# Optimization experiments

Measured on AMD Instinct MI355X. Metric: run time of the kernel, lower is better.

## Reference

```python
import jax, jax.numpy as jnp
import numpy as np

N, G, P = 512, 11560, 2000
E_SG, E_GP, E_PP = 1000000, 200000, 50000
HID, HEADS, L = 192, 4, 2
C = HID // HEADS
NQ, OUT = 20, 128
EPS = 1e-5


def setup_inputs():
    key = jax.random.key(0)
    ks = iter(jax.random.split(key, 64))
    def rn(shape, s=0.05):
        return jax.random.normal(next(ks), shape, jnp.float32) * s
    def ri(n, hi):
        return jax.random.randint(next(ks), (n,), 0, hi)
    return dict(
        x_sample=rn((N, HID), 1.0), x_gene=rn((G, HID), 1.0), x_pathway=rn((P, HID), 1.0),
        e_sg_src=ri(E_SG, N), e_sg_dst=ri(E_SG, G),
        e_gp_src=ri(E_GP, G), e_gp_dst=ri(E_GP, P),
        e_pp_src=ri(E_PP, P), e_pp_dst=ri(E_PP, P),
        sage_Wl=rn((L, 2, HID, HID)), sage_bl=jnp.zeros((L, 2, HID)), sage_Wr=rn((L, 2, HID, HID)),
        gat_Wl=rn((L, 3, HID, HID)), gat_bl=jnp.zeros((L, 3, HID)),
        gat_Wr=rn((L, 3, HID, HID)), gat_br=jnp.zeros((L, 3, HID)),
        gat_att=rn((L, 3, HEADS, C), 0.1), gat_bias=jnp.zeros((L, 3, HID)),
        ln_g=jnp.ones((L, 3, HID)), ln_b=jnp.zeros((L, 3, HID)),
        pool_query=rn((NQ, HID), 1.0),
        pool_in_w=rn((3 * HID, HID)), pool_in_b=jnp.zeros((3 * HID,)),
        pool_out_w=rn((HID, HID)), pool_out_b=jnp.zeros((HID,)),
        ff_w1=rn((HID, HID)), ff_b1=jnp.zeros((HID,)),
        ff_w2=rn((HID, HID)), ff_b2=jnp.zeros((HID,)),
        pool_ln_g=jnp.ones((HID,)), pool_ln_b=jnp.zeros((HID,)),
        proj_w=rn((OUT, HID)), proj_b=jnp.zeros((OUT,)),
    )


def _ln(x, g, b):
    mu = x.mean(-1, keepdims=True)
    v = ((x - mu) ** 2).mean(-1, keepdims=True)
    return (x - mu) / jnp.sqrt(v + EPS) * g + b


def _sage(x_src, x_dst, src, dst, Wl, bl, Wr, n_dst):
    # PyG SAGEConv: lin_l(mean_aggr(x_src[neighbors])) + lin_r(x_dst)
    s = jax.ops.segment_sum(x_src[src], dst, num_segments=n_dst)
    cnt = jax.ops.segment_sum(jnp.ones((src.shape[0],), x_src.dtype), dst, num_segments=n_dst)
    mean = s / jnp.maximum(cnt, 1.0)[:, None]
    return mean @ Wl.T + bl + x_dst @ Wr.T


def _gatv2(x_src, x_dst, src, dst, Wl, bl, Wr, br, att, bias, n_dst):
    # transform nodes first (cheap), then gather per edge
    gl = (x_src @ Wl.T + bl).reshape(-1, HEADS, C)[src]   # [E,H,C]
    gr = (x_dst @ Wr.T + br).reshape(-1, HEADS, C)[dst]   # [E,H,C]
    e = jax.nn.leaky_relu(gl + gr, 0.2)
    score = jnp.einsum('ehc,hc->eh', e, att)              # [E,H]
    m = jax.ops.segment_max(score, dst, num_segments=n_dst)
    ex = jnp.exp(score - m[dst])
    den = jax.ops.segment_sum(ex, dst, num_segments=n_dst)
    alpha = ex / (den[dst] + 1e-16)
    out = jax.ops.segment_sum(alpha[:, :, None] * gl, dst, num_segments=n_dst)
    return out.reshape(n_dst, HID) + bias


def reference(x_sample, x_gene, x_pathway, e_sg_src, e_sg_dst, e_gp_src, e_gp_dst,
              e_pp_src, e_pp_dst, sage_Wl, sage_bl, sage_Wr, gat_Wl, gat_bl, gat_Wr,
              gat_br, gat_att, gat_bias, ln_g, ln_b, pool_query, pool_in_w, pool_in_b,
              pool_out_w, pool_out_b, ff_w1, ff_b1, ff_w2, ff_b2, pool_ln_g, pool_ln_b,
              proj_w, proj_b):
    xs, xg, xp = x_sample, x_gene, x_pathway
    for l in range(L):
        og = _sage(xs, xg, e_sg_src, e_sg_dst, sage_Wl[l, 0], sage_bl[l, 0], sage_Wr[l, 0], G)
        os_ = _sage(xg, xs, e_sg_dst, e_sg_src, sage_Wl[l, 1], sage_bl[l, 1], sage_Wr[l, 1], N)
        op = _gatv2(xg, xp, e_gp_src, e_gp_dst, gat_Wl[l, 0], gat_bl[l, 0], gat_Wr[l, 0],
                    gat_br[l, 0], gat_att[l, 0], gat_bias[l, 0], P)
        og = og + _gatv2(xp, xg, e_gp_dst, e_gp_src, gat_Wl[l, 1], gat_bl[l, 1], gat_Wr[l, 1],
                         gat_br[l, 1], gat_att[l, 1], gat_bias[l, 1], G)
        op = op + _gatv2(xp, xp, e_pp_src, e_pp_dst, gat_Wl[l, 2], gat_bl[l, 2], gat_Wr[l, 2],
                         gat_br[l, 2], gat_att[l, 2], gat_bias[l, 2], P)
        # residual + LayerNorm (dropout = identity in eval)
        xs = _ln(xs + os_, ln_g[l, 0], ln_b[l, 0])
        xg = _ln(xg + og, ln_g[l, 1], ln_b[l, 1])
        xp = _ln(xp + op, ln_g[l, 2], ln_b[l, 2])
    # MultiQueryPooling over sample nodes (batch=1 MultiheadAttention)
    Wq, Wk, Wv = jnp.split(pool_in_w, 3, axis=0)
    bq, bk, bv = jnp.split(pool_in_b, 3, axis=0)
    q = (pool_query @ Wq.T + bq).reshape(NQ, HEADS, C)
    k = (xs @ Wk.T + bk).reshape(N, HEADS, C)
    v = (xs @ Wv.T + bv).reshape(N, HEADS, C)
    attn = jax.nn.softmax(jnp.einsum('qhc,nhc->hqn', q, k) / (C ** 0.5), axis=-1)
    o = jnp.einsum('hqn,nhc->qhc', attn, v).reshape(NQ, HID) @ pool_out_w.T + pool_out_b
    pooled = o.mean(0)  # [HID]
    h = jax.nn.relu(pooled @ ff_w1.T + ff_b1) @ ff_w2.T + ff_b2
    h = _ln(h, pool_ln_g, pool_ln_b)
    return (h @ proj_w.T + proj_b)[None, :]  # [1, OUT]
```

## Files before the change

### kernel.cpp

```cpp
#include <hip/hip_runtime.h>

#define N_S 512
#define N_G 11560
#define N_P 2000
#define NE_SG 1000000
#define NE_GP 200000
#define NE_PP 50000
#define HID 192
#define HEADS 4
#define CDIM 48
#define NQd 20
#define OUTD 128
#define LDK 12288
#define SPLITK 16
#define CHUNKK 768

typedef __attribute__((ext_vector_type(8))) short short8;
typedef __attribute__((ext_vector_type(4))) float float4v;

__device__ __forceinline__ float bf2f(unsigned short u){
  union { unsigned int i; float f; } x; x.i = ((unsigned int)u) << 16; return x.f;
}
__device__ __forceinline__ unsigned short f2bf(float f){
  union { float f; unsigned int i; } u; u.f = f;
  unsigned int r = u.i + 0x7FFFu + ((u.i >> 16) & 1u);
  return (unsigned short)(r >> 16);
}
__device__ __forceinline__ ushort4 f4bf(float4 v){
  return make_ushort4(f2bf(v.x), f2bf(v.y), f2bf(v.z), f2bf(v.w));
}

__global__ __launch_bounds__(256) void k_detect(const unsigned int* __restrict__ raw,
                                                int* __restrict__ flag){
  __shared__ int cnt;
  if (threadIdx.x == 0) cnt = 0;
  __syncthreads();
  int c = 0;
  for (int i = threadIdx.x; i < 2048; i += 256) {
    float f = __uint_as_float(raw[i]);
    float a = fabsf(f);
    if (f == f && a > 1e-4f && a < 1000.0f) c++;
  }
  atomicAdd(&cnt, c);
  __syncthreads();
  if (threadIdx.x == 0) flag[0] = (cnt >= 1024) ? 1 : 0;
}

#define NLOAD 27
#define LOADBX 2048
struct LoadDesc { const void* src; float* dst; int n; };
struct LoadTable { LoadDesc d[NLOAD]; };
__global__ __launch_bounds__(256)
void k_load_all(LoadTable tab, const int* __restrict__ flag){
  LoadDesc de = tab.d[blockIdx.y];
  int fp32 = flag[0];
  for (int i = blockIdx.x*256 + threadIdx.x; i < de.n; i += LOADBX*256) {
    if (fp32) de.dst[i] = ((const float*)de.src)[i];
    else      de.dst[i] = bf2f(((const unsigned short*)de.src)[i]);
  }
}

__global__ __launch_bounds__(256)
void k_cntbuild(const int* __restrict__ src, const int* __restrict__ dst,
                int* __restrict__ cg, int E){
  int i = blockIdx.x*256 + threadIdx.x;
  if (i >= E) return;
  atomicAdd(&cg[(size_t)dst[i]*N_S + src[i]], 1);
}

__global__ __launch_bounds__(256)
void k_cvtT(const int* __restrict__ cg, unsigned short* __restrict__ bfA,
            unsigned short* __restrict__ bfB){
  __shared__ unsigned short tile[64][68];
  int g0 = blockIdx.x*64, s0 = blockIdx.y*64;
  int t = threadIdx.x; int r = t>>2, seg = t&3;
  int g = g0 + r;
  if (g < N_G) {
    const int* row = cg + (size_t)g*N_S + s0 + seg*16;
    unsigned short* arow = bfA + (size_t)g*N_S + s0 + seg*16;
    #pragma unroll
    for (int i=0;i<16;i++){
      unsigned short v = f2bf((float)row[i]);
      tile[r][seg*16+i] = v;
      arow[i] = v;
    }
  } else {
    #pragma unroll
    for (int i=0;i<16;i++) tile[r][seg*16+i] = 0;
  }
  __syncthreads();
  int s = s0 + r;
  unsigned short* brow = bfB + (size_t)s*LDK + g0 + seg*16;
  #pragma unroll
  for (int i=0;i<16;i++) brow[i] = tile[seg*16+i][r];
}

__global__ __launch_bounds__(256)
void k_rowinv_i(const int* __restrict__ A, int lda, int cols, int n,
                float* __restrict__ outp){
  int row = blockIdx.x*4 + (threadIdx.x >> 6);
  if (row >= n) return;
  int lane = threadIdx.x & 63;
  const int* Ar = A + (size_t)row*lda;
  float s = 0.0f;
  for (int c = lane; c < cols; c += 64) s += (float)Ar[c];
  #pragma unroll
  for (int o = 32; o; o >>= 1) s += __shfl_xor(s, o);
  if (lane == 0) outp[row] = 1.0f / fmaxf(s, 1.0f);
}
__global__ __launch_bounds__(256)
void k_rowinv_h(const unsigned short* __restrict__ A, int lda, int cols, int n,
                float* __restrict__ outp){
  int row = blockIdx.x*4 + (threadIdx.x >> 6);
  if (row >= n) return;
  int lane = threadIdx.x & 63;
  const unsigned short* Ar = A + (size_t)row*lda;
  float s = 0.0f;
  for (int c = lane; c < cols; c += 64) s += bf2f(Ar[c]);
  #pragma unroll
  for (int o = 32; o; o >>= 1) s += __shfl_xor(s, o);
  if (lane == 0) outp[row] = 1.0f / fmaxf(s, 1.0f);
}

struct TransJobs { const float* inA; unsigned short* outA; int nA; int ldoA; int rbA;
                   const float* inB; unsigned short* outB; int nB; int ldoB; };
__global__ __launch_bounds__(256)
void k_transpose2(TransJobs tj){
  const float* in; unsigned short* outp; int n, ldo, r0;
  int bx = blockIdx.x;
  if (bx < tj.rbA) { in = tj.inA; outp = tj.outA; n = tj.nA; ldo = tj.ldoA; r0 = bx*64; }
  else             { in = tj.inB; outp = tj.outB; n = tj.nB; ldo = tj.ldoB; r0 = (bx - tj.rbA)*64; }
  __shared__ float tile[64][65];
  int c0 = blockIdx.y*64;
  int t = threadIdx.x;
  int r = t >> 2, seg = t & 3;
  int grr = r0 + r;
  if (grr < n) {
    #pragma unroll
    for (int i = 0; i < 4; i++) {
      float4 v = *(const float4*)(in + (size_t)grr*HID + c0 + seg*16 + i*4);
      tile[r][seg*16+i*4+0] = v.x; tile[r][seg*16+i*4+1] = v.y;
      tile[r][seg*16+i*4+2] = v.z; tile[r][seg*16+i*4+3] = v.w;
    }
  } else {
    #pragma unroll
    for (int i = 0; i < 16; i++) tile[r][seg*16+i] = 0.0f;
  }
  __syncthreads();
  int w = t >> 6, lane = t & 63;
  if (r0 + lane < ldo) {
    #pragma unroll
    for (int j = 0; j < 16; j++) {
      int c = w*16 + j;
      outp[(size_t)(c0+c)*ldo + r0 + lane] = f2bf(tile[lane][c]);
    }
  }
}

struct CsrJob { const int* src; const int* dst; int E; int n;
                int* deg; int* rowptr; int* cursor; int* col; };
struct CsrJobs { CsrJob j[3]; };

__global__ __launch_bounds__(256) void k_hist3(CsrJobs jobs){
  CsrJob jb = jobs.j[blockIdx.y];
  int i = blockIdx.x*256 + threadIdx.x;
  if (i < jb.E) atomicAdd(&jb.deg[jb.dst[i]], 1);
}
__global__ __launch_bounds__(256) void k_scan3(CsrJobs jobs){
  CsrJob jb = jobs.j[blockIdx.x];
  __shared__ int part[256];
  __shared__ int pre[256];
  int t = threadIdx.x;
  int n = jb.n;
  int C = (n + 255) >> 8;
  int lo = t*C, hi = min(n, lo + C);
  int s = 0;
  for (int i = lo; i < hi; i++) s += jb.deg[i];
  part[t] = s;
  __syncthreads();
  if (t == 0) {
    int acc = 0;
    for (int i = 0; i < 256; i++) { pre[i] = acc; acc += part[i]; }
    jb.rowptr[n] = acc;
  }
  __syncthreads();
  int run = pre[t];
  for (int i = lo; i < hi; i++) {
    jb.rowptr[i] = run; jb.cursor[i] = run; run += jb.deg[i];
  }
}
__global__ __launch_bounds__(256) void k_fill3(CsrJobs jobs){
  CsrJob jb = jobs.j[blockIdx.y];
  int i = blockIdx.x*256 + threadIdx.x;
  if (i >= jb.E) return;
  int pos = atomicAdd(&jb.cursor[jb.dst[i]], 1);
  jb.col[pos] = jb.src[i];
}

#define LDA 200
__global__ __launch_bounds__(256)
void k_gemm(const float* __restrict__ A, const float* __restrict__ rowscale,
            const float* __restrict__ W, const float* __restrict__ bias,
            float* __restrict__ outp, int n, int accum)
{
  __shared__ __align__(16) unsigned short Asm[64*LDA];
  __shared__ __align__(16) unsigned short Wsm[64*LDA];
  int t = threadIdx.x;
  int row0 = blockIdx.x * 64;
  int col0 = blockIdx.y * 64;
  {
    int r = t >> 2, seg = t & 3;
    int gr = row0 + r;
    unsigned short* ad = Asm + r*LDA + seg*48;
    if (gr < n) {
      float sc = rowscale ? rowscale[gr] : 1.0f;
      const float* Ar = A + (size_t)gr*HID + seg*48;
      #pragma unroll
      for (int i = 0; i < 12; i++) {
        float4 v = *reinterpret_cast<const float4*>(Ar + i*4);
        v.x *= sc; v.y *= sc; v.z *= sc; v.w *= sc;
        *reinterpret_cast<ushort4*>(ad + i*4) = f4bf(v);
      }
    } else {
      ushort4 z = make_ushort4(0,0,0,0);
      #pragma unroll
      for (int i = 0; i < 12; i++) *reinterpret_cast<ushort4*>(ad + i*4) = z;
    }
    const float* Wr = W + (size_t)(col0 + r)*HID + seg*48;
    unsigned short* wd = Wsm + r*LDA + seg*48;
    #pragma unroll
    for (int i = 0; i < 12; i++) {
      float4 v = *reinterpret_cast<const float4*>(Wr + i*4);
      *reinterpret_cast<ushort4*>(wd + i*4) = f4bf(v);
    }
  }
  __syncthreads();
  int w = t >> 6, lane = t & 63;
  int quad = lane >> 4, mr = lane & 15;
  float4v acc[4] = {};
  const unsigned short* Abase = Asm + (w*16 + mr)*LDA + quad*8;
  const unsigned short* Wbase = Wsm + mr*LDA + quad*8;
  #pragma unroll
  for (int k0 = 0; k0 < 6; k0++) {
    short8 a = *reinterpret_cast<const short8*>(Abase + k0*32);
    #pragma unroll
    for (int ct = 0; ct < 4; ct++) {
      short8 b = *reinterpret_cast<const short8*>(Wbase + ct*16*LDA + k0*32);
      acc[ct] = __builtin_amdgcn_mfma_f32_16x16x32_bf16(a, b, acc[ct], 0, 0, 0);
    }
  }
  #pragma unroll
  for (int ct = 0; ct < 4; ct++) {
    #pragma unroll
    for (int reg = 0; reg < 4; reg++) {
      int rr = row0 + w*16 + quad*4 + reg;
      if (rr < n) {
        int cc = col0 + ct*16 + mr;
        float v = acc[ct][reg];
        if (bias) v += bias[cc];
        if (accum) v += outp[(size_t)rr*HID + cc];
        outp[(size_t)rr*HID + cc] = v;
      }
    }
  }
}

struct GemmJob { const float* A; const float* W; const float* bias;
                 unsigned short* out; int n; };
struct GemmJobs { GemmJob j[6]; int rb[7]; };
__global__ __launch_bounds__(256)
void k_gemm6(GemmJobs jobs)
{
  int bx = blockIdx.x;
  int z = 0;
  #pragma unroll
  for (int q = 1; q < 6; q++) if (bx >= jobs.rb[q]) z = q;
  GemmJob jb = jobs.j[z];
  int row0 = (bx - jobs.rb[z]) * 64;
  __shared__ __align__(16) unsigned short Asm[64*LDA];
  __shared__ __align__(16) unsigned short Wsm[64*LDA];
  int t = threadIdx.x;
  int col0 = blockIdx.y * 64;
  {
    int r = t >> 2, seg = t & 3;
    int gr = row0 + r;
    unsigned short* ad = Asm + r*LDA + seg*48;
    if (gr < jb.n) {
      const float* Ar = jb.A + (size_t)gr*HID + seg*48;
      #pragma unroll
      for (int i = 0; i < 12; i++) {
        float4 v = *reinterpret_cast<const float4*>(Ar + i*4);
        *reinterpret_cast<ushort4*>(ad + i*4) = f4bf(v);
      }
    } else {
      ushort4 zz = make_ushort4(0,0,0,0);
      #pragma unroll
      for (int i = 0; i < 12; i++) *reinterpret_cast<ushort4*>(ad + i*4) = zz;
    }
    const float* Wr = jb.W + (size_t)(col0 + r)*HID + seg*48;
    unsigned short* wd = Wsm + r*LDA + seg*48;
    #pragma unroll
    for (int i = 0; i < 12; i++) {
      float4 v = *reinterpret_cast<const float4*>(Wr + i*4);
      *reinterpret_cast<ushort4*>(wd + i*4) = f4bf(v);
    }
  }
  __syncthreads();
  int w = t >> 6, lane = t & 63;
  int quad = lane >> 4, mr = lane & 15;
  float4v acc[4] = {};
  const unsigned short* Abase = Asm + (w*16 + mr)*LDA + quad*8;
  const unsigned short* Wbase = Wsm + mr*LDA + quad*8;
  #pragma unroll
  for (int k0 = 0; k0 < 6; k0++) {
    short8 a = *reinterpret_cast<const short8*>(Abase + k0*32);
    #pragma unroll
    for (int ct = 0; ct < 4; ct++) {
      short8 b = *reinterpret_cast<const short8*>(Wbase + ct*16*LDA + k0*32);
      acc[ct] = __builtin_amdgcn_mfma_f32_16x16x32_bf16(a, b, acc[ct], 0, 0, 0);
    }
  }
  #pragma unroll
  for (int ct = 0; ct < 4; ct++) {
    #pragma unroll
    for (int reg = 0; reg < 4; reg++) {
      int rr = row0 + w*16 + quad*4 + reg;
      if (rr < jb.n) {
        int cc = col0 + ct*16 + mr;
        jb.out[(size_t)rr*HID + cc] = f2bf(acc[ct][reg] + jb.bias[cc]);
      }
    }
  }
}

struct PoolJob { const float* A; const float* W; const float* bias;
                 float* out; int n; };
struct PoolJobs { PoolJob j[3]; int rb[4]; };
__global__ __launch_bounds__(256)
void k_gemm3(PoolJobs jobs)
{
  int bx = blockIdx.x;
  int z = 0;
  if (bx >= jobs.rb[1]) z = 1;
  if (bx >= jobs.rb[2]) z = 2;
  PoolJob jb = jobs.j[z];
  int row0 = (bx - jobs.rb[z]) * 64;
  __shared__ __align__(16) unsigned short Asm[64*LDA];
  __shared__ __align__(16) unsigned short Wsm[64*LDA];
  int t = threadIdx.x;
  int col0 = blockIdx.y * 64;
  {
    int r = t >> 2, seg = t & 3;
    int gr = row0 + r;
    unsigned short* ad = Asm + r*LDA + seg*48;
    if (gr < jb.n) {
      const float* Ar = jb.A + (size_t)gr*HID + seg*48;
      #pragma unroll
      for (int i = 0; i < 12; i++) {
        float4 v = *reinterpret_cast<const float4*>(Ar + i*4);
        *reinterpret_cast<ushort4*>(ad + i*4) = f4bf(v);
      }
    } else {
      ushort4 zz = make_ushort4(0,0,0,0);
      #pragma unroll
      for (int i = 0; i < 12; i++) *reinterpret_cast<ushort4*>(ad + i*4) = zz;
    }
    const float* Wr = jb.W + (size_t)(col0 + r)*HID + seg*48;
    unsigned short* wd = Wsm + r*LDA + seg*48;
    #pragma unroll
    for (int i = 0; i < 12; i++) {
      float4 v = *reinterpret_cast<const float4*>(Wr + i*4);
      *reinterpret_cast<ushort4*>(wd + i*4) = f4bf(v);
    }
  }
  __syncthreads();
  int w = t >> 6, lane = t & 63;
  int quad = lane >> 4, mr = lane & 15;
  float4v acc[4] = {};
  const unsigned short* Abase = Asm + (w*16 + mr)*LDA + quad*8;
  const unsigned short* Wbase = Wsm + mr*LDA + quad*8;
  #pragma unroll
  for (int k0 = 0; k0 < 6; k0++) {
    short8 a = *reinterpret_cast<const short8*>(Abase + k0*32);
    #pragma unroll
    for (int ct = 0; ct < 4; ct++) {
      short8 b = *reinterpret_cast<const short8*>(Wbase + ct*16*LDA + k0*32);
      acc[ct] = __builtin_amdgcn_mfma_f32_16x16x32_bf16(a, b, acc[ct], 0, 0, 0);
    }
  }
  #pragma unroll
  for (int ct = 0; ct < 4; ct++) {
    #pragma unroll
    for (int reg = 0; reg < 4; reg++) {
      int rr = row0 + w*16 + quad*4 + reg;
      if (rr < jb.n) {
        int cc = col0 + ct*16 + mr;
        jb.out[(size_t)rr*HID + cc] = acc[ct][reg] + jb.bias[cc];
      }
    }
  }
}

__global__ __launch_bounds__(256)
void k_gemm2(const float* __restrict__ A1, const float* __restrict__ rs1,
             const float* __restrict__ W1,
             const float* __restrict__ A2, const float* __restrict__ W2,
             const float* __restrict__ bias,
             float* __restrict__ outp, int n)
{
  __shared__ __align__(16) unsigned short Asm[64*LDA];
  __shared__ __align__(16) unsigned short Wsm[64*LDA];
  int t = threadIdx.x;
  int row0 = blockIdx.x * 64;
  int col0 = blockIdx.y * 64;
  int r = t >> 2, seg = t & 3;
  int w = t >> 6, lane = t & 63;
  int quad = lane >> 4, mr = lane & 15;
  float4v acc[4] = {};
  for (int p = 0; p < 2; p++) {
    if (p) __syncthreads();
    const float* A = p ? A2 : A1;
    const float* W = p ? W2 : W1;
    {
      int gr = row0 + r;
      unsigned short* ad = Asm + r*LDA + seg*48;
      if (gr < n) {
        float sc = (!p && rs1) ? rs1[gr] : 1.0f;
        const float* Ar = A + (size_t)gr*HID + seg*48;
        #pragma unroll
        for (int i = 0; i < 12; i++) {
          float4 v = *reinterpret_cast<const float4*>(Ar + i*4);
          v.x *= sc; v.y *= sc; v.z *= sc; v.w *= sc;
          *reinterpret_cast<ushort4*>(ad + i*4) = f4bf(v);
        }
      } else {
        ushort4 z = make_ushort4(0,0,0,0);
        #pragma unroll
        for (int i = 0; i < 12; i++) *reinterpret_cast<ushort4*>(ad + i*4) = z;
      }
      const float* Wr = W + (size_t)(col0 + r)*HID + seg*48;
      unsigned short* wd = Wsm + r*LDA + seg*48;
      #pragma unroll
      for (int i = 0; i < 12; i++) {
        float4 v = *reinterpret_cast<const float4*>(Wr + i*4);
        *reinterpret_cast<ushort4*>(wd + i*4) = f4bf(v);
      }
    }
    __syncthreads();
    const unsigned short* Abase = Asm + (w*16 + mr)*LDA + quad*8;
    const unsigned short* Wbase = Wsm + mr*LDA + quad*8;
    #pragma unroll
    for (int k0 = 0; k0 < 6; k0++) {
      short8 a = *reinterpret_cast<const short8*>(Abase + k0*32);
      #pragma unroll
      for (int ct = 0; ct < 4; ct++) {
        short8 b = *reinterpret_cast<const short8*>(Wbase + ct*16*LDA + k0*32);
        acc[ct] = __builtin_amdgcn_mfma_f32_16x16x32_bf16(a, b, acc[ct], 0, 0, 0);
      }
    }
  }
  #pragma unroll
  for (int ct = 0; ct < 4; ct++) {
    #pragma unroll
    for (int reg = 0; reg < 4; reg++) {
      int rr = row0 + w*16 + quad*4 + reg;
      if (rr < n) {
        int cc = col0 + ct*16 + mr;
        outp[(size_t)rr*HID + cc] = acc[ct][reg] + bias[cc];
      }
    }
  }
}

#define BKG 128
#define LDG 136
__global__ __launch_bounds__(256)
void k_gemm_g(const unsigned short* __restrict__ A, int lda,
              const unsigned short* __restrict__ W, int ldw,
              float* __restrict__ outp, int n, int K)
{
  __shared__ __align__(16) unsigned short Asm[64*LDG];
  __shared__ __align__(16) unsigned short Wsm[64*LDG];
  int t = threadIdx.x;
  int row0 = blockIdx.x * 64;
  int col0 = blockIdx.y * 64;
  int r = t >> 2, seg = t & 3;
  int w = t >> 6, lane = t & 63;
  int quad = lane >> 4, mr = lane & 15;
  float4v acc[4] = {};
  for (int k0 = 0; k0 < K; k0 += BKG) {
    {
      int gr = row0 + r;
      unsigned short* ad = Asm + r*LDG + seg*32;
      if (gr < n) {
        const unsigned short* Ar = A + (size_t)gr*lda + k0 + seg*32;
        #pragma unroll
        for (int i = 0; i < 4; i++) *(uint4*)(ad + i*8) = *(const uint4*)(Ar + i*8);
      } else {
        uint4 z = make_uint4(0,0,0,0);
        #pragma unroll
        for (int i = 0; i < 4; i++) *(uint4*)(ad + i*8) = z;
      }
      const unsigned short* Wr = W + (size_t)(col0 + r)*ldw + k0 + seg*32;
      unsigned short* wd = Wsm + r*LDG + seg*32;
      #pragma unroll
      for (int i = 0; i < 4; i++) *(uint4*)(wd + i*8) = *(const uint4*)(Wr + i*8);
    }
    __syncthreads();
    const unsigned short* Abase = Asm + (w*16 + mr)*LDG + quad*8;
    const unsigned short* Wbase = Wsm + mr*LDG + quad*8;
    #pragma unroll
    for (int kk = 0; kk < 4; kk++) {
      short8 a = *(const short8*)(Abase + kk*32);
      #pragma unroll
      for (int ct = 0; ct < 4; ct++) {
        short8 b = *(const short8*)(Wbase + ct*16*LDG + kk*32);
        acc[ct] = __builtin_amdgcn_mfma_f32_16x16x32_bf16(a, b, acc[ct], 0, 0, 0);
      }
    }
    __syncthreads();
  }
  #pragma unroll
  for (int ct = 0; ct < 4; ct++) {
    #pragma unroll
    for (int reg = 0; reg < 4; reg++) {
      int rr = row0 + w*16 + quad*4 + reg;
      if (rr < n) outp[(size_t)rr*HID + col0 + ct*16 + mr] = acc[ct][reg];
    }
  }
}

__global__ __launch_bounds__(256)
void k_gemm_sk(const unsigned short* __restrict__ A, int lda,
               const unsigned short* __restrict__ W, int ldw,
               float* __restrict__ part, int n)
{
  __shared__ __align__(16) unsigned short Asm[64*LDG];
  __shared__ __align__(16) unsigned short Wsm[64*LDG];
  int t = threadIdx.x;
  int row0 = blockIdx.x * 64;
  int col0 = blockIdx.y * 64;
  int kz   = blockIdx.z;
  int kbeg = kz * CHUNKK;
  int r = t >> 2, seg = t & 3;
  int w = t >> 6, lane = t & 63;
  int quad = lane >> 4, mr = lane & 15;
  float4v acc[4] = {};
  for (int k0 = kbeg; k0 < kbeg + CHUNKK; k0 += BKG) {
    {
      int gr = row0 + r;
      unsigned short* ad = Asm + r*LDG + seg*32;
      if (gr < n) {
        const unsigned short* Ar = A + (size_t)gr*lda + k0 + seg*32;
        #pragma unroll
        for (int i = 0; i < 4; i++) *(uint4*)(ad + i*8) = *(const uint4*)(Ar + i*8);
      } else {
        uint4 z = make_uint4(0,0,0,0);
        #pragma unroll
        for (int i = 0; i < 4; i++) *(uint4*)(ad + i*8) = z;
      }
      const unsigned short* Wr = W + (size_t)(col0 + r)*ldw + k0 + seg*32;
      unsigned short* wd = Wsm + r*LDG + seg*32;
      #pragma unroll
      for (int i = 0; i < 4; i++) *(uint4*)(wd + i*8) = *(const uint4*)(Wr + i*8);
    }
    __syncthreads();
    const unsigned short* Abase = Asm + (w*16 + mr)*LDG + quad*8;
    const unsigned short* Wbase = Wsm + mr*LDG + quad*8;
    #pragma unroll
    for (int kk = 0; kk < 4; kk++) {
      short8 a = *(const short8*)(Abase + kk*32);
      #pragma unroll
      for (int ct = 0; ct < 4; ct++) {
        short8 b = *(const short8*)(Wbase + ct*16*LDG + kk*32);
        acc[ct] = __builtin_amdgcn_mfma_f32_16x16x32_bf16(a, b, acc[ct], 0, 0, 0);
      }
    }
    __syncthreads();
  }
  float* pd = part + (size_t)kz*n*HID;
  #pragma unroll
  for (int ct = 0; ct < 4; ct++) {
    #pragma unroll
    for (int reg = 0; reg < 4; reg++) {
      int rr = row0 + w*16 + quad*4 + reg;
      if (rr < n) pd[(size_t)rr*HID + col0 + ct*16 + mr] = acc[ct][reg];
    }
  }
}

__global__ __launch_bounds__(256)
void k_reduce_sk(const float* __restrict__ part, float* __restrict__ outp, int n){
  int i = blockIdx.x*256 + threadIdx.x;
  if (i >= n*HID) return;
  float s = 0.0f;
  #pragma unroll
  for (int z = 0; z < SPLITK; z++) s += part[(size_t)z*n*HID + i];
  outp[i] = s;
}

struct GatJob { const unsigned short* gl; const unsigned short* gr;
                const int* rowptr; const int* col;
                const float* att; const float* bias; float* out; int ndst; int accum; };
struct GatJobs { GatJob j[3]; int bo[4]; };

__global__ __launch_bounds__(256)
void k_gat_all(GatJobs jobs)
{
  int bx = blockIdx.x;
  int jz = 0;
  if (bx >= jobs.bo[1]) jz = 1;
  if (bx >= jobs.bo[2]) jz = 2;
  GatJob jb = jobs.j[jz];
  int tid = threadIdx.x;
  int w = tid >> 6, lane = tid & 63;
  int dst = (bx - jobs.bo[jz])*4 + w;
  bool active = dst < jb.ndst;
  __shared__ float attS[HID];
  __shared__ float grS[4][HID];
  __shared__ float swS[4][4][16];
  __shared__ int   sidxS[4][16];
  __shared__ float fS[4][4];
  __shared__ float lS[4][4];
  if (tid < HID) attS[tid] = jb.att[tid];
  if (active) {
    const unsigned short* grr = jb.gr + (size_t)dst*HID;
    grS[w][lane]     = bf2f(grr[lane]);
    grS[w][lane+64]  = bf2f(grr[lane+64]);
    grS[w][lane+128] = bf2f(grr[lane+128]);
  }
  __syncthreads();
  if (!active) return;

  int h16 = lane >> 4, j16 = lane & 15;
  int start = jb.rowptr[dst], end = jb.rowptr[dst+1];
  float m = -1e30f, l = 0.0f;
  float acc0 = 0.f, acc1 = 0.f, acc2 = 0.f;
  int hd0 = lane/48, hd1 = (lane+64)/48, hd2 = (lane+128)/48;
  const float* attH = attS + h16*CDIM;
  const float* grH  = grS[w] + h16*CDIM;

  for (int c0 = start; c0 < end; c0 += 16) {
    int nc = min(16, end - c0);
    float sc = -1e30f; int s = -1;
    if (j16 < nc) {
      s = jb.col[c0 + j16];
      const short8* glv = (const short8*)(jb.gl + (size_t)s*HID + h16*CDIM);
      float a = 0.0f;
      #pragma unroll
      for (int v8 = 0; v8 < 6; v8++) {
        short8 g8 = glv[v8];
        #pragma unroll
        for (int jj = 0; jj < 8; jj++) {
          float v = bf2f((unsigned short)g8[jj]) + grH[v8*8+jj];
          v = v > 0.0f ? v : 0.2f*v;
          a += v * attH[v8*8+jj];
        }
      }
      sc = a;
    }
    if (h16 == 0) sidxS[w][j16] = s;
    float cm = sc;
    cm = fmaxf(cm, __shfl_xor(cm, 1));
    cm = fmaxf(cm, __shfl_xor(cm, 2));
    cm = fmaxf(cm, __shfl_xor(cm, 4));
    cm = fmaxf(cm, __shfl_xor(cm, 8));
    float nm = fmaxf(m, cm);
    float f = __expf(m - nm);
    l *= f;
    float e = (j16 < nc) ? __expf(sc - nm) : 0.0f;
    swS[w][h16][j16] = e;
    float cl = e;
    cl += __shfl_xor(cl, 1);
    cl += __shfl_xor(cl, 2);
    cl += __shfl_xor(cl, 4);
    cl += __shfl_xor(cl, 8);
    l += cl;
    m = nm;
    if (j16 == 0) fS[w][h16] = f;
    acc0 *= fS[w][hd0]; acc1 *= fS[w][hd1]; acc2 *= fS[w][hd2];
    for (int j = 0; j < nc; j++) {
      const unsigned short* glr = jb.gl + (size_t)sidxS[w][j]*HID;
      acc0 += swS[w][hd0][j] * bf2f(glr[lane]);
      acc1 += swS[w][hd1][j] * bf2f(glr[lane+64]);
      acc2 += swS[w][hd2][j] * bf2f(glr[lane+128]);
    }
  }
  if (j16 == 0) lS[w][h16] = l;
  float* od = jb.out + (size_t)dst*HID;
  float v0 = acc0 / (lS[w][hd0] + 1e-16f) + jb.bias[lane];
  float v1 = acc1 / (lS[w][hd1] + 1e-16f) + jb.bias[lane+64];
  float v2 = acc2 / (lS[w][hd2] + 1e-16f) + jb.bias[lane+128];
  if (jb.accum) { v0 += od[lane]; v1 += od[lane+64]; v2 += od[lane+128]; }
  od[lane] = v0; od[lane+64] = v1; od[lane+128] = v2;
}

__global__ __launch_bounds__(64)
void k_ln3(float* __restrict__ xs, const float* __restrict__ osb,
           float* __restrict__ xg, const float* __restrict__ og,
           float* __restrict__ xp, const float* __restrict__ opb,
           const float* __restrict__ op2,
           const float* __restrict__ LNg, const float* __restrict__ LNb, int l)
{
  int r = blockIdx.x;
  float* x; const float* d1; const float* d2 = nullptr; int typ;
  if (r < N_S)            { x = xs + (size_t)r*HID; d1 = osb + (size_t)r*HID; typ = 0; }
  else if (r < N_S + N_G) { int rr = r - N_S; x = xg + (size_t)rr*HID; d1 = og + (size_t)rr*HID; typ = 1; }
  else                    { int rr = r - N_S - N_G; x = xp + (size_t)rr*HID; d1 = opb + (size_t)rr*HID;
                            d2 = op2 + (size_t)rr*HID; typ = 2; }
  const float* g = LNg + (l*3 + typ)*HID;
  const float* b = LNb + (l*3 + typ)*HID;
  int lane = threadIdx.x;
  float v[3]; float sum = 0.0f;
  #pragma unroll
  for (int j=0;j<3;j++){
    int d = j*64 + lane;
    float t = x[d] + d1[d];
    if (d2) t += d2[d];
    v[j] = t; sum += t;
  }
  #pragma unroll
  for (int o=32;o;o>>=1) sum += __shfl_xor(sum, o);
  float mu = sum * (1.0f/HID);
  float var = 0.0f;
  #pragma unroll
  for (int j=0;j<3;j++){ float dd = v[j]-mu; var += dd*dd; }
  #pragma unroll
  for (int o=32;o;o>>=1) var += __shfl_xor(var, o);
  var *= (1.0f/HID);
  float inv = rsqrtf(var + 1e-5f);
  #pragma unroll
  for (int j=0;j<3;j++){
    int d = j*64 + lane;
    x[d] = (v[j]-mu)*inv*g[d] + b[d];
  }
}

__global__ __launch_bounds__(256)
void k_pool_attn(const float* __restrict__ qb, const float* __restrict__ kb,
                 const float* __restrict__ vb, float* __restrict__ ob)
{
  int h = blockIdx.x & 3;
  int q = blockIdx.x >> 2;
  __shared__ float prob[N_S];
  __shared__ float red[256];
  int t = threadIdx.x;
  const float* qrow = qb + (size_t)q*HID + h*CDIM;
  const float scale = 0.14433756729740643f;
  for (int n = t; n < N_S; n += 256) {
    const float* krow = kb + (size_t)n*HID + h*CDIM;
    float s = 0.0f;
    #pragma unroll 8
    for (int c=0;c<CDIM;c++) s += qrow[c]*krow[c];
    prob[n] = s * scale;
  }
  __syncthreads();
  float m = -1e30f;
  for (int n=t;n<N_S;n+=256) m = fmaxf(m, prob[n]);
  red[t] = m; __syncthreads();
  for (int s2=128;s2;s2>>=1){ if (t<s2) red[t]=fmaxf(red[t],red[t+s2]); __syncthreads(); }
  m = red[0]; __syncthreads();
  float sum = 0.0f;
  for (int n=t;n<N_S;n+=256){ float e=__expf(prob[n]-m); prob[n]=e; sum+=e; }
  red[t] = sum; __syncthreads();
  for (int s2=128;s2;s2>>=1){ if (t<s2) red[t]+=red[t+s2]; __syncthreads(); }
  float inv = 1.0f/red[0];
  __syncthreads();
  if (t < CDIM) {
    float acc = 0.0f;
    for (int n=0;n<N_S;n++) acc += prob[n]*vb[(size_t)n*HID + h*CDIM + t];
    ob[(size_t)q*HID + h*CDIM + t] = acc * inv;
  }
}

__global__ __launch_bounds__(192)
void k_tail(const float* __restrict__ ob2,
            const float* ffw1, const float* ffb1,
            const float* ffw2, const float* ffb2,
            const float* lng, const float* lnb,
            const float* pw, const float* pb,
            void* __restrict__ outp, const int* __restrict__ flag)
{
  __shared__ float pooled[HID];
  __shared__ float hh[HID];
  __shared__ float stats[2];
  int t = threadIdx.x;
  float a = 0.0f;
  for (int q=0;q<NQd;q++) a += ob2[q*HID + t];
  pooled[t] = a * (1.0f/NQd);
  __syncthreads();
  float s1 = ffb1[t];
  for (int k=0;k<HID;k++) s1 += pooled[k]*ffw1[t*HID+k];
  hh[t] = fmaxf(s1, 0.0f);
  __syncthreads();
  float s2 = ffb2[t];
  for (int k=0;k<HID;k++) s2 += hh[k]*ffw2[t*HID+k];
  __syncthreads();
  hh[t] = s2;
  __syncthreads();
  if (t == 0) {
    float mu=0.0f; for (int k=0;k<HID;k++) mu += hh[k];
    mu *= (1.0f/HID);
    float v=0.0f; for (int k=0;k<HID;k++){ float d=hh[k]-mu; v+=d*d; }
    v *= (1.0f/HID);
    stats[0]=mu; stats[1]=rsqrtf(v + 1e-5f);
  }
  __syncthreads();
  pooled[t] = (hh[t]-stats[0])*stats[1]*lng[t] + lnb[t];
  __syncthreads();
  if (t < OUTD) {
    float acc = pb[t];
    for (int k=0;k<HID;k++) acc += pooled[k]*pw[t*HID+k];
    if (flag[0]) ((float*)outp)[t] = acc;
    else         ((unsigned short*)outp)[t] = f2bf(acc);
  }
}

extern "C" void kernel_launch(void* const* d_in, const int* in_sizes, int n_in,
                              void* d_out, int out_size, void* d_ws, size_t ws_size,
                              hipStream_t stream)
{
  const int* sg_src = (const int*)d_in[3];
  const int* sg_dst = (const int*)d_in[4];
  const int* gp_src = (const int*)d_in[5];
  const int* gp_dst = (const int*)d_in[6];
  const int* pp_src = (const int*)d_in[7];
  const int* pp_dst = (const int*)d_in[8];

  float* base = (float*)d_ws;
  size_t off = 0;
  auto alloc = [&](size_t nf){ nf = (nf + 3) & ~(size_t)3; float* p = base + off; off += nf; return p; };
  int*   flag = (int*)alloc(4);
  float* xs   = alloc((size_t)N_S*HID);
  float* xg   = alloc((size_t)N_G*HID);
  float* xp   = alloc((size_t)N_P*HID);
  float* qin  = alloc((size_t)NQd*HID);
  float* Wsl  = alloc(2*2*HID*HID); float* bsl = alloc(2*2*HID); float* Wsr = alloc(2*2*HID*HID);
  float* Wgl  = alloc(2*3*HID*HID); float* bgl = alloc(2*3*HID);
  float* Wgr  = alloc(2*3*HID*HID); float* bgr = alloc(2*3*HID);
  float* Agat = alloc(2*3*HEADS*CDIM); float* Bgat = alloc(2*3*HID);
  float* LNg  = alloc(2*3*HID); float* LNb = alloc(2*3*HID);
  float* Pinw = alloc(3*HID*HID); float* Pinb = alloc(3*HID);
  float* Poutw= alloc(HID*HID);   float* Poutb= alloc(HID);
  float* Fw1  = alloc(HID*HID);   float* Fb1  = alloc(HID);
  float* Fw2  = alloc(HID*HID);   float* Fb2  = alloc(HID);
  float* PLg  = alloc(HID);       float* PLb  = alloc(HID);
  float* Pw   = alloc(OUTD*HID);  float* Pb   = alloc(OUTD);
  float* agg  = alloc((size_t)N_G*HID);
  float* aggS = alloc((size_t)N_S*HID);
  float* og   = alloc((size_t)N_G*HID);
  float* osb  = alloc((size_t)N_S*HID);
  float* opb  = alloc((size_t)N_P*HID);
  float* op2  = alloc((size_t)N_P*HID);
  unsigned short* glGb  = (unsigned short*)alloc((size_t)N_G*HID/2);
  unsigned short* grGb  = (unsigned short*)alloc((size_t)N_G*HID/2);
  unsigned short* grP0b = (unsigned short*)alloc((size_t)N_P*HID/2);
  unsigned short* glP1b = (unsigned short*)alloc((size_t)N_P*HID/2);
  unsigned short* glP2b = (unsigned short*)alloc((size_t)N_P*HID/2);
  unsigned short* grP2b = (unsigned short*)alloc((size_t)N_P*HID/2);
  float* qbuf = alloc((size_t)NQd*HID);
  float* kbuf = alloc((size_t)N_S*HID);
  float* vbuf = alloc((size_t)N_S*HID);
  float* obuf = alloc((size_t)NQd*HID);
  float* ob2  = alloc((size_t)NQd*HID);
  int*            CntGi = (int*)alloc((size_t)N_G*N_S);
  unsigned short* CntGb = (unsigned short*)alloc((size_t)N_G*N_S/2);
  unsigned short* CntSb = (unsigned short*)alloc((size_t)N_S*LDK/2);
  unsigned short* xsTb  = (unsigned short*)alloc((size_t)HID*N_S/2);
  unsigned short* xgTb  = (unsigned short*)alloc((size_t)HID*LDK/2);
  float* part = alloc((size_t)SPLITK*N_S*HID);
  float* invdegG = alloc(N_G);
  float* invdegS = alloc(N_S);
  int* degAll = (int*)alloc(2*N_P + N_G + 4);
  int* curAll = (int*)alloc(2*N_P + N_G + 4);
  int* rp_gp_p = (int*)alloc(N_P+2);  int* col_gp_p = (int*)alloc(NE_GP);
  int* rp_gp_g = (int*)alloc(N_G+2);  int* col_gp_g = (int*)alloc(NE_GP);
  int* rp_pp_p = (int*)alloc(N_P+2);  int* col_pp_p = (int*)alloc(NE_PP);
  (void)ws_size; (void)in_sizes; (void)n_in; (void)out_size;

  k_detect<<<1,256,0,stream>>>((const unsigned int*)d_in[0], flag);

  {
    LoadTable tab;
    int k = 0;
    auto add = [&](int i, float* dst, int n){ tab.d[k].src = d_in[i]; tab.d[k].dst = dst; tab.d[k].n = n; k++; };
    add(0,  xs,  N_S*HID);  add(1,  xg,  N_G*HID);  add(2,  xp,  N_P*HID);
    add(9,  Wsl, 2*2*HID*HID); add(10, bsl, 2*2*HID); add(11, Wsr, 2*2*HID*HID);
    add(12, Wgl, 2*3*HID*HID); add(13, bgl, 2*3*HID);
    add(14, Wgr, 2*3*HID*HID); add(15, bgr, 2*3*HID);
    add(16, Agat, 2*3*HEADS*CDIM); add(17, Bgat, 2*3*HID);
    add(18, LNg, 2*3*HID); add(19, LNb, 2*3*HID);
    add(20, qin, NQd*HID);
    add(21, Pinw, 3*HID*HID); add(22, Pinb, 3*HID);
    add(23, Poutw, HID*HID);  add(24, Poutb, HID);
    add(25, Fw1, HID*HID); add(26, Fb1, HID);
    add(27, Fw2, HID*HID); add(28, Fb2, HID);
    add(29, PLg, HID); add(30, PLb, HID);
    add(31, Pw, OUTD*HID); add(32, Pb, OUTD);
    k_load_all<<<dim3(LOADBX, NLOAD),256,0,stream>>>(tab, flag);
  }

  hipMemsetAsync(CntGi, 0, (size_t)N_G*N_S*4, stream);
  hipMemsetAsync(degAll, 0, (size_t)(2*N_P + N_G)*4, stream);
  k_cntbuild<<<(NE_SG+255)/256,256,0,stream>>>(sg_src, sg_dst, CntGi, NE_SG);
  k_cvtT<<<dim3(LDK/64, N_S/64),256,0,stream>>>(CntGi, CntGb, CntSb);
  k_rowinv_i<<<(N_G+3)/4,256,0,stream>>>(CntGi, N_S, N_S, N_G, invdegG);
  k_rowinv_h<<<(N_S+3)/4,256,0,stream>>>(CntSb, LDK, LDK, N_S, invdegS);

  {
    CsrJobs jobs;
    jobs.j[0] = { gp_src, gp_dst, NE_GP, N_P, degAll,           rp_gp_p, curAll,           col_gp_p };
    jobs.j[1] = { gp_dst, gp_src, NE_GP, N_G, degAll+N_P,       rp_gp_g, curAll+N_P,       col_gp_g };
    jobs.j[2] = { pp_src, pp_dst, NE_PP, N_P, degAll+N_P+N_G,   rp_pp_p, curAll+N_P+N_G,   col_pp_p };
    k_hist3<<<dim3((NE_GP+255)/256, 3),256,0,stream>>>(jobs);
    k_scan3<<<3,256,0,stream>>>(jobs);
    k_fill3<<<dim3((NE_GP+255)/256, 3),256,0,stream>>>(jobs);
  }

  const int RB_G = (N_G+63)/64, RB_P = (N_P+63)/64;
  const int GB_P = (N_P+3)/4,  GB_G = (N_G+3)/4;

  for (int l=0; l<2; l++) {
    {
      TransJobs tj;
      tj.inA = xs; tj.outA = xsTb; tj.nA = N_S; tj.ldoA = N_S; tj.rbA = 8;
      tj.inB = xg; tj.outB = xgTb; tj.nB = N_G; tj.ldoB = LDK;
      k_transpose2<<<dim3(8 + LDK/64, 3),256,0,stream>>>(tj);
    }
    k_gemm_g<<<dim3(RB_G,3),256,0,stream>>>(CntGb, N_S, xsTb, N_S, agg, N_G, N_S);
    k_gemm2<<<dim3(RB_G,3),256,0,stream>>>(agg, invdegG,
        Wsl + (size_t)(l*2+0)*HID*HID, xg, Wsr + (size_t)(l*2+0)*HID*HID,
        bsl + (l*2+0)*HID, og, N_G);

    k_gemm_sk<<<dim3(8,3,SPLITK),256,0,stream>>>(CntSb, LDK, xgTb, LDK, part, N_S);
    k_reduce_sk<<<(N_S*HID+255)/256,256,0,stream>>>(part, aggS, N_S);
    k_gemm2<<<dim3((N_S+63)/64,3),256,0,stream>>>(aggS, invdegS,
        Wsl + (size_t)(l*2+1)*HID*HID, xs, Wsr + (size_t)(l*2+1)*HID*HID,
        bsl + (l*2+1)*HID, osb, N_S);

    {
      GemmJobs gj;
      int w0 = l*3+0, w1 = l*3+1, w2 = l*3+2;
      gj.j[0] = { xg, Wgl + (size_t)w0*HID*HID, bgl + w0*HID, glGb,  N_G };
      gj.j[1] = { xp, Wgr + (size_t)w0*HID*HID, bgr + w0*HID, grP0b, N_P };
      gj.j[2] = { xp, Wgl + (size_t)w1*HID*HID, bgl + w1*HID, glP1b, N_P };
      gj.j[3] = { xg, Wgr + (size_t)w1*HID*HID, bgr + w1*HID, grGb,  N_G };
      gj.j[4] = { xp, Wgl + (size_t)w2*HID*HID, bgl + w2*HID, glP2b, N_P };
      gj.j[5] = { xp, Wgr + (size_t)w2*HID*HID, bgr + w2*HID, grP2b, N_P };
      int nrb[6] = { RB_G, RB_P, RB_P, RB_G, RB_P, RB_P };
      gj.rb[0] = 0;
      for (int q = 0; q < 6; q++) gj.rb[q+1] = gj.rb[q] + nrb[q];
      k_gemm6<<<dim3(gj.rb[6],3),256,0,stream>>>(gj);
    }
    {
      GatJobs gt;
      int w0 = l*3+0, w1 = l*3+1, w2 = l*3+2;
      gt.j[0] = { glGb,  grP0b, rp_gp_p, col_gp_p, Agat + (size_t)w0*HID, Bgat + (size_t)w0*HID, opb, N_P, 0 };
      gt.j[1] = { glP1b, grGb,  rp_gp_g, col_gp_g, Agat + (size_t)w1*HID, Bgat + (size_t)w1*HID, og,  N_G, 1 };
      gt.j[2] = { glP2b, grP2b, rp_pp_p, col_pp_p, Agat + (size_t)w2*HID, Bgat + (size_t)w2*HID, op2, N_P, 0 };
      gt.bo[0] = 0; gt.bo[1] = GB_P; gt.bo[2] = GB_P + GB_G; gt.bo[3] = GB_P + GB_G + GB_P;
      k_gat_all<<<dim3(gt.bo[3]),256,0,stream>>>(gt);
    }
    k_ln3<<<N_S+N_G+N_P,64,0,stream>>>(xs, osb, xg, og, xp, opb, op2, LNg, LNb, l);
  }

  {
    PoolJobs pj;
    pj.j[0] = { qin, Pinw,                     Pinb,         qbuf, NQd };
    pj.j[1] = { xs,  Pinw + (size_t)HID*HID,   Pinb + HID,   kbuf, N_S };
    pj.j[2] = { xs,  Pinw + (size_t)2*HID*HID, Pinb + 2*HID, vbuf, N_S };
    pj.rb[0] = 0; pj.rb[1] = 1; pj.rb[2] = 1 + (N_S+63)/64; pj.rb[3] = pj.rb[2] + (N_S+63)/64;
    k_gemm3<<<dim3(pj.rb[3],3),256,0,stream>>>(pj);
  }
  k_pool_attn<<<NQd*HEADS,256,0,stream>>>(qbuf, kbuf, vbuf, obuf);
  k_gemm<<<dim3(1,3),256,0,stream>>>(obuf, nullptr, Poutw, Poutb, ob2, NQd, 0);
  k_tail<<<1,HID,0,stream>>>(ob2, Fw1, Fb1, Fw2, Fb2, PLg, PLb, Pw, Pb, d_out, flag);
}
```

Measured before the change: 730.7 us.

## Batch SAGE GEMM launches into grouped kernels and cache GAT gathers in LDS

The gene-side aggregation GEMM and the 16 split-K sample-side GEMMs now run in one grouped launch that uses per-block job tables. The two SAGE combine GEMMs are merged into one launch the same way. This is meant to cut launch count and let small jobs share the GPU. In the GAT kernel, the gathered neighbor features are stored in shared memory during the score pass, so the aggregation pass reads them from LDS instead of gathering from global memory a second time. The cost is extra LDS per block, which may lower occupancy, plus a 17-way job lookup loop per block.

```diff
diff --git a/kernel.cpp b/kernel.cpp
--- a/kernel.cpp
+++ b/kernel.cpp
@@ -199,9 +199,9 @@
 
 #define LDA 200
 __global__ __launch_bounds__(256)
-void k_gemm(const float* __restrict__ A, const float* __restrict__ rowscale,
+void k_gemm(const float* __restrict__ A,
             const float* __restrict__ W, const float* __restrict__ bias,
-            float* __restrict__ outp, int n, int accum)
+            float* __restrict__ outp, int n)
 {
   __shared__ __align__(16) unsigned short Asm[64*LDA];
   __shared__ __align__(16) unsigned short Wsm[64*LDA];
@@ -213,12 +213,10 @@
     int gr = row0 + r;
     unsigned short* ad = Asm + r*LDA + seg*48;
     if (gr < n) {
-      float sc = rowscale ? rowscale[gr] : 1.0f;
       const float* Ar = A + (size_t)gr*HID + seg*48;
       #pragma unroll
       for (int i = 0; i < 12; i++) {
         float4 v = *reinterpret_cast<const float4*>(Ar + i*4);
-        v.x *= sc; v.y *= sc; v.z *= sc; v.w *= sc;
         *reinterpret_cast<ushort4*>(ad + i*4) = f4bf(v);
       }
     } else {
@@ -256,10 +254,7 @@
       int rr = row0 + w*16 + quad*4 + reg;
       if (rr < n) {
         int cc = col0 + ct*16 + mr;
-        float v = acc[ct][reg];
-        if (bias) v += bias[cc];
-        if (accum) v += outp[(size_t)rr*HID + cc];
-        outp[(size_t)rr*HID + cc] = v;
+        outp[(size_t)rr*HID + cc] = acc[ct][reg] + bias[cc];
       }
     }
   }
@@ -401,17 +396,20 @@
   }
 }
 
-__global__ __launch_bounds__(256)
-void k_gemm2(const float* __restrict__ A1, const float* __restrict__ rs1,
-             const float* __restrict__ W1,
-             const float* __restrict__ A2, const float* __restrict__ W2,
-             const float* __restrict__ bias,
-             float* __restrict__ outp, int n)
+struct G2Job { const float* A1; const float* rs1; const float* W1;
+               const float* A2; const float* W2; const float* bias;
+               float* out; int n; };
+struct G2Jobs { G2Job j[2]; int rb[3]; };
+__global__ __launch_bounds__(256)
+void k_gemm2(G2Jobs jobs)
 {
+  int bx = blockIdx.x;
+  int z = (bx >= jobs.rb[1]) ? 1 : 0;
+  G2Job jb = jobs.j[z];
+  int row0 = (bx - jobs.rb[z]) * 64;
   __shared__ __align__(16) unsigned short Asm[64*LDA];
   __shared__ __align__(16) unsigned short Wsm[64*LDA];
   int t = threadIdx.x;
-  int row0 = blockIdx.x * 64;
   int col0 = blockIdx.y * 64;
   int r = t >> 2, seg = t & 3;
   int w = t >> 6, lane = t & 63;
@@ -419,13 +417,13 @@
   float4v acc[4] = {};
   for (int p = 0; p < 2; p++) {
     if (p) __syncthreads();
-    const float* A = p ? A2 : A1;
-    const float* W = p ? W2 : W1;
+    const float* A = p ? jb.A2 : jb.A1;
+    const float* W = p ? jb.W2 : jb.W1;
     {
       int gr = row0 + r;
       unsigned short* ad = Asm + r*LDA + seg*48;
-      if (gr < n) {
-        float sc = (!p && rs1) ? rs1[gr] : 1.0f;
+      if (gr < jb.n) {
+        float sc = (!p && jb.rs1) ? jb.rs1[gr] : 1.0f;
         const float* Ar = A + (size_t)gr*HID + seg*48;
         #pragma unroll
         for (int i = 0; i < 12; i++) {
@@ -434,9 +432,9 @@
           *reinterpret_cast<ushort4*>(ad + i*4) = f4bf(v);
         }
       } else {
-        ushort4 z = make_ushort4(0,0,0,0);
+        ushort4 zz = make_ushort4(0,0,0,0);
         #pragma unroll
-        for (int i = 0; i < 12; i++) *reinterpret_cast<ushort4*>(ad + i*4) = z;
+        for (int i = 0; i < 12; i++) *reinterpret_cast<ushort4*>(ad + i*4) = zz;
       }
       const float* Wr = W + (size_t)(col0 + r)*HID + seg*48;
       unsigned short* wd = Wsm + r*LDA + seg*48;
@@ -464,9 +462,9 @@
     #pragma unroll
     for (int reg = 0; reg < 4; reg++) {
       int rr = row0 + w*16 + quad*4 + reg;
-      if (rr < n) {
+      if (rr < jb.n) {
         int cc = col0 + ct*16 + mr;
-        outp[(size_t)rr*HID + cc] = acc[ct][reg] + bias[cc];
+        jb.out[(size_t)rr*HID + cc] = acc[ct][reg] + jb.bias[cc];
       }
     }
   }
@@ -474,34 +472,40 @@
 
 #define BKG 128
 #define LDG 136
-__global__ __launch_bounds__(256)
-void k_gemm_g(const unsigned short* __restrict__ A, int lda,
-              const unsigned short* __restrict__ W, int ldw,
-              float* __restrict__ outp, int n, int K)
+struct KJob { const unsigned short* A; int lda;
+              const unsigned short* W; int ldw;
+              float* out; int n; int kbeg; int kend; };
+struct KJobs { KJob j[17]; int rb[18]; };
+__global__ __launch_bounds__(256)
+void k_gemm_k(KJobs jobs)
 {
+  int bx = blockIdx.x;
+  int z = 0;
+  for (int q = 1; q < 17; q++) if (bx >= jobs.rb[q]) z = q;
+  KJob jb = jobs.j[z];
+  int row0 = (bx - jobs.rb[z]) * 64;
   __shared__ __align__(16) unsigned short Asm[64*LDG];
   __shared__ __align__(16) unsigned short Wsm[64*LDG];
   int t = threadIdx.x;
-  int row0 = blockIdx.x * 64;
   int col0 = blockIdx.y * 64;
   int r = t >> 2, seg = t & 3;
   int w = t >> 6, lane = t & 63;
   int quad = lane >> 4, mr = lane & 15;
   float4v acc[4] = {};
-  for (int k0 = 0; k0 < K; k0 += BKG) {
+  for (int k0 = jb.kbeg; k0 < jb.kend; k0 += BKG) {
     {
       int gr = row0 + r;
       unsigned short* ad = Asm + r*LDG + seg*32;
-      if (gr < n) {
-        const unsigned short* Ar = A + (size_t)gr*lda + k0 + seg*32;
+      if (gr < jb.n) {
+        const unsigned short* Ar = jb.A + (size_t)gr*jb.lda + k0 + seg*32;
         #pragma unroll
         for (int i = 0; i < 4; i++) *(uint4*)(ad + i*8) = *(const uint4*)(Ar + i*8);
       } else {
-        uint4 z = make_uint4(0,0,0,0);
+        uint4 zz = make_uint4(0,0,0,0);
         #pragma unroll
-        for (int i = 0; i < 4; i++) *(uint4*)(ad + i*8) = z;
-      }
-      const unsigned short* Wr = W + (size_t)(col0 + r)*ldw + k0 + seg*32;
+        for (int i = 0; i < 4; i++) *(uint4*)(ad + i*8) = zz;
+      }
+      const unsigned short* Wr = jb.W + (size_t)(col0 + r)*jb.ldw + k0 + seg*32;
       unsigned short* wd = Wsm + r*LDG + seg*32;
       #pragma unroll
       for (int i = 0; i < 4; i++) *(uint4*)(wd + i*8) = *(const uint4*)(Wr + i*8);
@@ -525,66 +529,7 @@
     #pragma unroll
     for (int reg = 0; reg < 4; reg++) {
       int rr = row0 + w*16 + quad*4 + reg;
-      if (rr < n) outp[(size_t)rr*HID + col0 + ct*16 + mr] = acc[ct][reg];
-    }
-  }
-}
-
-__global__ __launch_bounds__(256)
-void k_gemm_sk(const unsigned short* __restrict__ A, int lda,
-               const unsigned short* __restrict__ W, int ldw,
-               float* __restrict__ part, int n)
-{
-  __shared__ __align__(16) unsigned short Asm[64*LDG];
-  __shared__ __align__(16) unsigned short Wsm[64*LDG];
-  int t = threadIdx.x;
-  int row0 = blockIdx.x * 64;
-  int col0 = blockIdx.y * 64;
-  int kz   = blockIdx.z;
-  int kbeg = kz * CHUNKK;
-  int r = t >> 2, seg = t & 3;
-  int w = t >> 6, lane = t & 63;
-  int quad = lane >> 4, mr = lane & 15;
-  float4v acc[4] = {};
-  for (int k0 = kbeg; k0 < kbeg + CHUNKK; k0 += BKG) {
-    {
-      int gr = row0 + r;
-      unsigned short* ad = Asm + r*LDG + seg*32;
-      if (gr < n) {
-        const unsigned short* Ar = A + (size_t)gr*lda + k0 + seg*32;
-        #pragma unroll
-        for (int i = 0; i < 4; i++) *(uint4*)(ad + i*8) = *(const uint4*)(Ar + i*8);
-      } else {
-        uint4 z = make_uint4(0,0,0,0);
-        #pragma unroll
-        for (int i = 0; i < 4; i++) *(uint4*)(ad + i*8) = z;
-      }
-      const unsigned short* Wr = W + (size_t)(col0 + r)*ldw + k0 + seg*32;
-      unsigned short* wd = Wsm + r*LDG + seg*32;
-      #pragma unroll
-      for (int i = 0; i < 4; i++) *(uint4*)(wd + i*8) = *(const uint4*)(Wr + i*8);
-    }
-    __syncthreads();
-    const unsigned short* Abase = Asm + (w*16 + mr)*LDG + quad*8;
-    const unsigned short* Wbase = Wsm + mr*LDG + quad*8;
-    #pragma unroll
-    for (int kk = 0; kk < 4; kk++) {
-      short8 a = *(const short8*)(Abase + kk*32);
-      #pragma unroll
-      for (int ct = 0; ct < 4; ct++) {
-        short8 b = *(const short8*)(Wbase + ct*16*LDG + kk*32);
-        acc[ct] = __builtin_amdgcn_mfma_f32_16x16x32_bf16(a, b, acc[ct], 0, 0, 0);
-      }
-    }
-    __syncthreads();
-  }
-  float* pd = part + (size_t)kz*n*HID;
-  #pragma unroll
-  for (int ct = 0; ct < 4; ct++) {
-    #pragma unroll
-    for (int reg = 0; reg < 4; reg++) {
-      int rr = row0 + w*16 + quad*4 + reg;
-      if (rr < n) pd[(size_t)rr*HID + col0 + ct*16 + mr] = acc[ct][reg];
+      if (rr < jb.n) jb.out[(size_t)rr*HID + col0 + ct*16 + mr] = acc[ct][reg];
     }
   }
 }
@@ -604,6 +549,7 @@
                 const float* att; const float* bias; float* out; int ndst; int accum; };
 struct GatJobs { GatJob j[3]; int bo[4]; };
 
+#define GLS_LD 200
 __global__ __launch_bounds__(256)
 void k_gat_all(GatJobs jobs)
 {
@@ -618,8 +564,8 @@
   bool active = dst < jb.ndst;
   __shared__ float attS[HID];
   __shared__ float grS[4][HID];
+  __shared__ __align__(16) unsigned short glS[4][16][GLS_LD];
   __shared__ float swS[4][4][16];
-  __shared__ int   sidxS[4][16];
   __shared__ float fS[4][4];
   __shared__ float lS[4][4];
   if (tid < HID) attS[tid] = jb.att[tid];
@@ -642,14 +588,16 @@
 
   for (int c0 = start; c0 < end; c0 += 16) {
     int nc = min(16, end - c0);
-    float sc = -1e30f; int s = -1;
+    float sc = -1e30f;
     if (j16 < nc) {
-      s = jb.col[c0 + j16];
+      int s = jb.col[c0 + j16];
       const short8* glv = (const short8*)(jb.gl + (size_t)s*HID + h16*CDIM);
+      unsigned short* ls = &glS[w][j16][h16*CDIM];
       float a = 0.0f;
       #pragma unroll
       for (int v8 = 0; v8 < 6; v8++) {
         short8 g8 = glv[v8];
+        *(short8*)(ls + v8*8) = g8;
         #pragma unroll
         for (int jj = 0; jj < 8; jj++) {
           float v = bf2f((unsigned short)g8[jj]) + grH[v8*8+jj];
@@ -659,7 +607,6 @@
       }
       sc = a;
     }
-    if (h16 == 0) sidxS[w][j16] = s;
     float cm = sc;
     cm = fmaxf(cm, __shfl_xor(cm, 1));
     cm = fmaxf(cm, __shfl_xor(cm, 2));
@@ -680,10 +627,9 @@
     if (j16 == 0) fS[w][h16] = f;
     acc0 *= fS[w][hd0]; acc1 *= fS[w][hd1]; acc2 *= fS[w][hd2];
     for (int j = 0; j < nc; j++) {
-      const unsigned short* glr = jb.gl + (size_t)sidxS[w][j]*HID;
-      acc0 += swS[w][hd0][j] * bf2f(glr[lane]);
-      acc1 += swS[w][hd1][j] * bf2f(glr[lane+64]);
-      acc2 += swS[w][hd2][j] * bf2f(glr[lane+128]);
+      acc0 += swS[w][hd0][j] * bf2f(glS[w][j][lane]);
+      acc1 += swS[w][hd1][j] * bf2f(glS[w][j][lane+64]);
+      acc2 += swS[w][hd2][j] * bf2f(glS[w][j][lane+128]);
     }
   }
   if (j16 == 0) lS[w][h16] = l;
@@ -927,17 +873,27 @@
       tj.inB = xg; tj.outB = xgTb; tj.nB = N_G; tj.ldoB = LDK;
       k_transpose2<<<dim3(8 + LDK/64, 3),256,0,stream>>>(tj);
     }
-    k_gemm_g<<<dim3(RB_G,3),256,0,stream>>>(CntGb, N_S, xsTb, N_S, agg, N_G, N_S);
-    k_gemm2<<<dim3(RB_G,3),256,0,stream>>>(agg, invdegG,
-        Wsl + (size_t)(l*2+0)*HID*HID, xg, Wsr + (size_t)(l*2+0)*HID*HID,
-        bsl + (l*2+0)*HID, og, N_G);
-
-    k_gemm_sk<<<dim3(8,3,SPLITK),256,0,stream>>>(CntSb, LDK, xgTb, LDK, part, N_S);
+    {
+      KJobs kj;
+      kj.j[0] = { CntGb, N_S, xsTb, N_S, agg, N_G, 0, N_S };
+      kj.rb[0] = 0; kj.rb[1] = RB_G;
+      for (int z = 0; z < SPLITK; z++) {
+        kj.j[1+z] = { CntSb, LDK, xgTb, LDK, part + (size_t)z*N_S*HID, N_S,
+                      z*CHUNKK, (z+1)*CHUNKK };
+        kj.rb[2+z] = kj.rb[1+z] + 8;
+      }
+      k_gemm_k<<<dim3(kj.rb[17],3),256,0,stream>>>(kj);
+    }
     k_reduce_sk<<<(N_S*HID+255)/256,256,0,stream>>>(part, aggS, N_S);
-    k_gemm2<<<dim3((N_S+63)/64,3),256,0,stream>>>(aggS, invdegS,
-        Wsl + (size_t)(l*2+1)*HID*HID, xs, Wsr + (size_t)(l*2+1)*HID*HID,
-        bsl + (l*2+1)*HID, osb, N_S);
-
+    {
+      G2Jobs g2;
+      g2.j[0] = { agg,  invdegG, Wsl + (size_t)(l*2+0)*HID*HID,
+                  xg, Wsr + (size_t)(l*2+0)*HID*HID, bsl + (l*2+0)*HID, og,  N_G };
+      g2.j[1] = { aggS, invdegS, Wsl + (size_t)(l*2+1)*HID*HID,
+                  xs, Wsr + (size_t)(l*2+1)*HID*HID, bsl + (l*2+1)*HID, osb, N_S };
+      g2.rb[0] = 0; g2.rb[1] = RB_G; g2.rb[2] = RB_G + (N_S+63)/64;
+      k_gemm2<<<dim3(g2.rb[2],3),256,0,stream>>>(g2);
+    }
     {
       GemmJobs gj;
       int w0 = l*3+0, w1 = l*3+1, w2 = l*3+2;
@@ -973,6 +929,6 @@
     k_gemm3<<<dim3(pj.rb[3],3),256,0,stream>>>(pj);
   }
   k_pool_attn<<<NQd*HEADS,256,0,stream>>>(qbuf, kbuf, vbuf, obuf);
-  k_gemm<<<dim3(1,3),256,0,stream>>>(obuf, nullptr, Poutw, Poutb, ob2, NQd, 0);
+  k_gemm<<<dim3(1,3),256,0,stream>>>(obuf, Poutw, Poutb, ob2, NQd);
   k_tail<<<1,HID,0,stream>>>(ob2, Fw1, Fb1, Fw2, Fb2, PLg, PLb, Pw, Pb, d_out, flag);
 }
```

After: 688.3 us. 1.06x faster.
